# Kernel optimization log

Measured on AMD Instinct MI355X. Metric: run time of the kernel, lower is better.

## Reference

```python
import jax, jax.numpy as jnp
import numpy as np

B, N, M = 4, 50000, 256
BIN_MIN, BIN_MAX = -3.0, 3.0


def setup_inputs() -> dict:
    key = jax.random.key(0)
    kx, ky = jax.random.split(key)
    x_coords = jax.random.normal(kx, (B, N), dtype=jnp.float32)
    y_coords = jax.random.normal(ky, (B, N), dtype=jnp.float32)
    bins = jnp.linspace(BIN_MIN, BIN_MAX, M, dtype=jnp.float32)
    return {"x_coords": x_coords, "y_coords": y_coords, "bins": bins}


def reference(x_coords, y_coords, bins):
    # bandwidth defaults to bin resolution (bins[1] - bins[0])
    bandwidth = bins[1] - bins[0]
    # per-axis Gaussian kernel values: (B, N, M)
    kx = jnp.exp(-0.5 * jnp.square((x_coords[..., None] - bins) / bandwidth))
    ky = jnp.exp(-0.5 * jnp.square((y_coords[..., None] - bins) / bandwidth))
    # joint kernel values reduced over particles: (B, M, M)
    joint = jnp.einsum("bni,bnj->bij", kx, ky)
    norm = jnp.sum(joint, axis=(-2, -1), keepdims=True) + 1e-10
    return joint / norm
```

## Files before the change

kernel.cpp:

```cpp
#include <hip/hip_runtime.h>


#define B_     4
#define N_     50000
#define M_     256
#define BK     64
#define NCH    48
#define KSTEPS 17
#define KCH    (KSTEPS * BK)
#define LDKB   80
#define ROWS   129
#define AXB    (ROWS * LDKB)
#define BUFB   (2 * AXB)
#define BLOCK  256
#define WINB   7
#define CS2    0.72134752f
#define HINV   0.36787944f

#if __has_builtin(__builtin_amdgcn_exp2f)
  #define EXP2(t) __builtin_amdgcn_exp2f(t)
#else
  #define EXP2(t) exp2f(t)
#endif

typedef __attribute__((ext_vector_type(4))) int i32x4;

__device__ __forceinline__ unsigned short bf16ru(float f) {
    return (unsigned short)((__builtin_bit_cast(unsigned, f) + 0x8000u) >> 16);
}
__device__ __forceinline__ float bf2f(unsigned short u) {
    return __builtin_bit_cast(float, ((unsigned)u) << 16);
}

template<int MT, int R0, bool SCAT>
__device__ __forceinline__ float chunk_loop(
    char* __restrict__ tb, const float* __restrict__ coord,
    int k0, int rowlo, int colbase, float bin0, float invbw,
    int ilo, int jlo, int wj, int lm, int quad, int tid,
    unsigned short* __restrict__ pb)
{
    i32x4 acc[MT][4];
    #pragma unroll
    for (int mt = 0; mt < MT; ++mt)
        #pragma unroll
        for (int nt = 0; nt < 4; ++nt) acc[mt][nt] = i32x4{0, 0, 0, 0};

    int ps0 = 1 << 20, ps1 = 1 << 20;

    float v0 = 3.0e30f, vnext = 3.0e30f;
    if (SCAT) {
        const int kcol = tid & 63;
        const int ka = k0 + kcol;       if (ka  < N_) v0    = coord[ka];
        const int kb2 = k0 + BK + kcol; if (kb2 < N_) vnext = coord[kb2];
    }
    __syncthreads();

    if (SCAT) {
        const float u  = (v0 - bin0) * invbw;
        const float st = rintf(u) - 3.0f;
        const float d0 = u - st;
        float E = 127.0f * EXP2(-CS2 * d0 * d0);
        float G = EXP2(fmaf(d0 + d0, CS2, -CS2));
        int rr = (int)st - rowlo;
        ps0 = rr;
        const int dmp = colbase + 128 * LDKB;
        #pragma unroll
        for (int j = 0; j < WINB; ++j) {
            tb[((unsigned)rr < 128u) ? (colbase + rr * LDKB) : dmp] =
                (char)(int)(E + 0.5f);
            E *= G; G *= HINV; ++rr;
        }
    }
    __syncthreads();

    for (int ks = 0; ks < KSTEPS; ++ks) {
        const int q = ks & 1;
        float vpre = 3.0e30f;
        if (SCAT && (ks + 2) < KSTEPS) {
            const int ka = k0 + (ks + 2) * BK + (tid & 63);
            if (ka < N_) vpre = coord[ka];
        }
        if (SCAT && (ks + 1) < KSTEPS) {
            const int qn  = q ^ 1;
            const int bqn = qn * BUFB + colbase;
            const int dmp = bqn + 128 * LDKB;
            const int ps  = qn ? ps1 : ps0;
            if (ps < (1 << 19)) {
                #pragma unroll
                for (int j = 0; j < WINB; ++j) {
                    const int rr = ps + j;
                    tb[((unsigned)rr < 128u) ? (bqn + rr * LDKB) : dmp] = 0;
                }
            }
            const float u  = (vnext - bin0) * invbw;
            const float st = rintf(u) - 3.0f;
            const float d0 = u - st;
            float E = 127.0f * EXP2(-CS2 * d0 * d0);
            float G = EXP2(fmaf(d0 + d0, CS2, -CS2));
            int rr = (int)st - rowlo;
            if (qn) ps1 = rr; else ps0 = rr;
            #pragma unroll
            for (int j = 0; j < WINB; ++j) {
                tb[((unsigned)rr < 128u) ? (bqn + rr * LDKB) : dmp] =
                    (char)(int)(E + 0.5f);
                E *= G; G *= HINV; ++rr;
            }
        }
        vnext = vpre;

        const char* bufA = tb + q * BUFB;
        const char* bufB = tb + q * BUFB + AXB;
        i32x4 af[MT], bfr[4];
        #pragma unroll
        for (int t4 = 0; t4 < MT; ++t4)
            af[t4] = *(const i32x4*)(bufA + (R0 + t4 * 16 + lm) * LDKB + quad * 16);
        #pragma unroll
        for (int t4 = 0; t4 < 4; ++t4)
            bfr[t4] = *(const i32x4*)(bufB + (wj + t4 * 16 + lm) * LDKB + quad * 16);
        #pragma unroll
        for (int mt = 0; mt < MT; ++mt)
            #pragma unroll
            for (int nt = 0; nt < 4; ++nt)
                acc[mt][nt] = __builtin_amdgcn_mfma_i32_16x16x64_i8(
                    af[mt], bfr[nt], acc[mt][nt], 0, 0, 0);
        __syncthreads();
    }

    float tsum = 0.f;
    #pragma unroll
    for (int mt = 0; mt < MT; ++mt) {
        const int row0 = ilo + R0 + mt * 16 + quad * 4;
        #pragma unroll
        for (int nt = 0; nt < 4; ++nt) {
            const int col = jlo + wj + nt * 16 + lm;
            const i32x4 a = acc[mt][nt];
            #pragma unroll
            for (int e = 0; e < 4; ++e) {
                const float v = (float)a[e];
                pb[(size_t)(row0 + e) * M_ + col] = bf16ru(v);
                tsum += v;
            }
        }
    }
    return tsum;
}

__global__ __launch_bounds__(BLOCK) void kde_gemm(
    const float* __restrict__ xs, const float* __restrict__ ys,
    const float* __restrict__ bins, unsigned short* __restrict__ partial,
    float* __restrict__ ws2, int wide)
{
    __shared__ __align__(16) char tiles[2][2][ROWS][LDKB];
    __shared__ float sred[4];

    const int tid   = threadIdx.x;
    const int tile  = blockIdx.x;
    const int chunk = blockIdx.y;
    const int b     = blockIdx.z;

    const int ilo = (tile & 1) * 128;
    const int jlo = (tile >> 1) * 128;
    const float bin0  = bins[0];
    const float invbw = 1.0f / (bins[1] - bin0);

    {
        int4* za = (int4*)&tiles[0][0][0][0];
        const int4 z4 = {0, 0, 0, 0};
        for (int t = tid; t < (int)(sizeof(tiles) / 16); t += BLOCK) za[t] = z4;
    }

    const int  axis    = (tid >> 6) & 1;
    const int  rowlo   = axis ? jlo : ilo;
    const int  colbase = axis * AXB + (tid & 63);
    const float* coord = (axis ? ys : xs) + b * N_;
    const int  k0 = chunk * KCH;
    char* const tb = &tiles[0][0][0][0];

    const int w    = tid >> 6;
    const int wj   = (w & 1) * 64;
    const int lane = tid & 63;
    const int lm   = lane & 15;
    const int quad = lane >> 4;
    unsigned short* pb = partial + (((size_t)chunk * B_ + b) << 16);

    float tsum;
    if (w < 2)
        tsum = chunk_loop<3, 0, true >(tb, coord, k0, rowlo, colbase, bin0, invbw,
                                       ilo, jlo, wj, lm, quad, tid, pb);
    else
        tsum = chunk_loop<5, 48, false>(tb, coord, k0, rowlo, colbase, bin0, invbw,
                                       ilo, jlo, wj, lm, quad, tid, pb);

    #pragma unroll
    for (int off = 32; off; off >>= 1) tsum += __shfl_xor(tsum, off);
    if (lane == 0) sred[w] = tsum;
    __syncthreads();
    if (tid == 0) {
        const float bsum = sred[0] + sred[1] + sred[2] + sred[3];
        if (wide) {
            const int bid = (b * NCH + chunk) * 4 + tile;
            ws2[bid] = bsum;
        } else {
            atomicAdd(&ws2[b], bsum);
        }
    }
}

__global__ __launch_bounds__(BLOCK) void kde_tail(
    const unsigned short* __restrict__ partial, const float* __restrict__ ws2,
    float* __restrict__ out, int wide)
{
    __shared__ float sred[4];
    __shared__ float snorm;
    const int tid = threadIdx.x;
    const int cellIdx = blockIdx.x * BLOCK + tid;
    const int bb = cellIdx >> 14;
    const int cb = cellIdx & 16383;

    float nrm;
    if (wide) {
        float t = (tid < 4 * NCH) ? ws2[bb * 4 * NCH + tid] : 0.f;
        #pragma unroll
        for (int off = 32; off; off >>= 1) t += __shfl_xor(t, off);
        if ((tid & 63) == 0) sred[tid >> 6] = t;
        __syncthreads();
        if (tid == 0) snorm = sred[0] + sred[1] + sred[2] + sred[3];
        __syncthreads();
        nrm = snorm;
    } else {
        nrm = ws2[bb];
    }

    float4 a = {0.f, 0.f, 0.f, 0.f};
    #pragma unroll 4
    for (int c = 0; c < NCH; ++c) {
        const ushort4 v = *(const ushort4*)(partial +
            (((size_t)c * B_ + bb) << 16) + (size_t)cb * 4);
        a.x += bf2f(v.x); a.y += bf2f(v.y); a.z += bf2f(v.z); a.w += bf2f(v.w);
    }
    const float sc = 1.0f / (nrm + 1e-10f);
    a.x *= sc; a.y *= sc; a.z *= sc; a.w *= sc;
    ((float4*)out)[cellIdx] = a;
}

extern "C" void kernel_launch(void* const* d_in, const int* in_sizes, int n_in,
                              void* d_out, int out_size, void* d_ws, size_t ws_size,
                              hipStream_t stream)
{
    const float* xs   = (const float*)d_in[0];
    const float* ys   = (const float*)d_in[1];
    const float* bins = (const float*)d_in[2];
    float* out = (float*)d_out;
    unsigned short* partial = (unsigned short*)d_ws;
    const size_t PSZ = (size_t)NCH * B_ * M_ * M_ * sizeof(unsigned short);
    float* ws2 = (float*)((char*)d_ws + PSZ);

    const int wide = (ws_size >= PSZ + 4096) ? 1 : 0;
    if (!wide) hipMemsetAsync(ws2, 0, 4 * sizeof(float), stream);

    kde_gemm<<<dim3(4, NCH, B_), dim3(BLOCK), 0, stream>>>(
        xs, ys, bins, partial, ws2, wide);
    kde_tail<<<dim3(B_ * M_ * M_ / (4 * BLOCK)), dim3(BLOCK), 0, stream>>>(
        partial, ws2, out, wide);
}
```

Measured before the change: 89.46 us.

## Widen GEMM block to 128x256 output tile with 8 waves and more K-chunks

Each block now computes a 128x256 slab of the joint histogram with 512 threads (8 waves, each doing a 64x64 sub-tile), instead of 128x128 tiles with 256 threads. Two waves still scatter the Gaussian window values into LDS for the x rows and the full y axis, so the x-side scatter is shared across twice as many output columns. NCH rises to 64 and KSTEPS drops to 13, giving more, shorter chunks. The cost is a larger partial-sum buffer that the tail kernel must reduce, plus bigger LDS use per block.

```diff
diff --git a/kernel.cpp b/kernel.cpp
--- a/kernel.cpp
+++ b/kernel.cpp
@@ -5,14 +5,16 @@
 #define N_     50000
 #define M_     256
 #define BK     64
-#define NCH    48
-#define KSTEPS 17
+#define NCH    64
+#define KSTEPS 13
 #define KCH    (KSTEPS * BK)
 #define LDKB   80
-#define ROWS   129
-#define AXB    (ROWS * LDKB)
-#define BUFB   (2 * AXB)
-#define BLOCK  256
+#define AROWS  128
+#define BROWS  256
+#define AXA    ((AROWS + 1) * LDKB)
+#define AXBB   ((BROWS + 1) * LDKB)
+#define BUFB   (AXA + AXBB)
+#define BLOCK  512
 #define WINB   7
 #define CS2    0.72134752f
 #define HINV   0.36787944f
@@ -32,30 +34,61 @@
     return __builtin_bit_cast(float, ((unsigned)u) << 16);
 }
 
-template<int MT, int R0, bool SCAT>
-__device__ __forceinline__ float chunk_loop(
-    char* __restrict__ tb, const float* __restrict__ coord,
-    int k0, int rowlo, int colbase, float bin0, float invbw,
-    int ilo, int jlo, int wj, int lm, int quad, int tid,
-    unsigned short* __restrict__ pb)
+__global__ __launch_bounds__(BLOCK, 4) void kde_gemm(
+    const float* __restrict__ xs, const float* __restrict__ ys,
+    const float* __restrict__ bins, unsigned short* __restrict__ partial,
+    float* __restrict__ ws2, int wide)
 {
-    i32x4 acc[MT][4];
+    __shared__ __align__(16) char tiles[2 * BUFB];
+    __shared__ float sred[8];
+
+    const int tid   = threadIdx.x;
+    const int itile = blockIdx.x;
+    const int chunk = blockIdx.y;
+    const int b     = blockIdx.z;
+
+    const int ilo = itile * 128;
+    const float bin0  = bins[0];
+    const float invbw = 1.0f / (bins[1] - bin0);
+
+    {
+        int4* za = (int4*)tiles;
+        const int4 z4 = {0, 0, 0, 0};
+        for (int t = tid; t < (2 * BUFB) / 16; t += BLOCK) za[t] = z4;
+    }
+
+    const int w    = tid >> 6;
+    const int lane = tid & 63;
+    const int lm   = lane & 15;
+    const int quad = lane >> 4;
+
+    const bool sc      = (w < 2);
+    const int  rowlo   = (w == 0) ? ilo : 0;
+    const unsigned clip = (w == 0) ? 128u : 256u;
+    const int  cb0     = ((w == 0) ? 0 : AXA) + lane;
+    const float* coord = ((w == 0) ? xs : ys) + b * N_;
+    const int  k0      = chunk * KCH;
+    char* const tb     = tiles;
+
+    const int R0 = (w >> 2) * 64;
+    const int wj = (w & 3) * 64;
+
+    i32x4 acc[4][4];
     #pragma unroll
-    for (int mt = 0; mt < MT; ++mt)
+    for (int mt = 0; mt < 4; ++mt)
         #pragma unroll
         for (int nt = 0; nt < 4; ++nt) acc[mt][nt] = i32x4{0, 0, 0, 0};
 
     int ps0 = 1 << 20, ps1 = 1 << 20;
 
     float v0 = 3.0e30f, vnext = 3.0e30f;
-    if (SCAT) {
-        const int kcol = tid & 63;
-        const int ka = k0 + kcol;       if (ka  < N_) v0    = coord[ka];
-        const int kb2 = k0 + BK + kcol; if (kb2 < N_) vnext = coord[kb2];
+    if (sc) {
+        const int ka = k0 + lane;       if (ka  < N_) v0    = coord[ka];
+        const int kb2 = k0 + BK + lane; if (kb2 < N_) vnext = coord[kb2];
     }
     __syncthreads();
 
-    if (SCAT) {
+    if (sc) {
         const float u  = (v0 - bin0) * invbw;
         const float st = rintf(u) - 3.0f;
         const float d0 = u - st;
@@ -63,10 +96,10 @@
         float G = EXP2(fmaf(d0 + d0, CS2, -CS2));
         int rr = (int)st - rowlo;
         ps0 = rr;
-        const int dmp = colbase + 128 * LDKB;
+        const int dmp = cb0 + (int)clip * LDKB;
         #pragma unroll
         for (int j = 0; j < WINB; ++j) {
-            tb[((unsigned)rr < 128u) ? (colbase + rr * LDKB) : dmp] =
+            tb[((unsigned)rr < clip) ? (cb0 + rr * LDKB) : dmp] =
                 (char)(int)(E + 0.5f);
             E *= G; G *= HINV; ++rr;
         }
@@ -76,20 +109,20 @@
     for (int ks = 0; ks < KSTEPS; ++ks) {
         const int q = ks & 1;
         float vpre = 3.0e30f;
-        if (SCAT && (ks + 2) < KSTEPS) {
-            const int ka = k0 + (ks + 2) * BK + (tid & 63);
+        if (sc && (ks + 2) < KSTEPS) {
+            const int ka = k0 + (ks + 2) * BK + lane;
             if (ka < N_) vpre = coord[ka];
         }
-        if (SCAT && (ks + 1) < KSTEPS) {
+        if (sc && (ks + 1) < KSTEPS) {
             const int qn  = q ^ 1;
-            const int bqn = qn * BUFB + colbase;
-            const int dmp = bqn + 128 * LDKB;
+            const int bqn = qn * BUFB + cb0;
+            const int dmp = bqn + (int)clip * LDKB;
             const int ps  = qn ? ps1 : ps0;
             if (ps < (1 << 19)) {
                 #pragma unroll
                 for (int j = 0; j < WINB; ++j) {
                     const int rr = ps + j;
-                    tb[((unsigned)rr < 128u) ? (bqn + rr * LDKB) : dmp] = 0;
+                    tb[((unsigned)rr < clip) ? (bqn + rr * LDKB) : dmp] = 0;
                 }
             }
             const float u  = (vnext - bin0) * invbw;
@@ -101,7 +134,7 @@
             if (qn) ps1 = rr; else ps0 = rr;
             #pragma unroll
             for (int j = 0; j < WINB; ++j) {
-                tb[((unsigned)rr < 128u) ? (bqn + rr * LDKB) : dmp] =
+                tb[((unsigned)rr < clip) ? (bqn + rr * LDKB) : dmp] =
                     (char)(int)(E + 0.5f);
                 E *= G; G *= HINV; ++rr;
             }
@@ -109,16 +142,16 @@
         vnext = vpre;
 
         const char* bufA = tb + q * BUFB;
-        const char* bufB = tb + q * BUFB + AXB;
-        i32x4 af[MT], bfr[4];
-        #pragma unroll
-        for (int t4 = 0; t4 < MT; ++t4)
+        const char* bufB = tb + q * BUFB + AXA;
+        i32x4 af[4], bfr[4];
+        #pragma unroll
+        for (int t4 = 0; t4 < 4; ++t4)
             af[t4] = *(const i32x4*)(bufA + (R0 + t4 * 16 + lm) * LDKB + quad * 16);
         #pragma unroll
         for (int t4 = 0; t4 < 4; ++t4)
             bfr[t4] = *(const i32x4*)(bufB + (wj + t4 * 16 + lm) * LDKB + quad * 16);
         #pragma unroll
-        for (int mt = 0; mt < MT; ++mt)
+        for (int mt = 0; mt < 4; ++mt)
             #pragma unroll
             for (int nt = 0; nt < 4; ++nt)
                 acc[mt][nt] = __builtin_amdgcn_mfma_i32_16x16x64_i8(
@@ -127,78 +160,35 @@
     }
 
     float tsum = 0.f;
-    #pragma unroll
-    for (int mt = 0; mt < MT; ++mt) {
-        const int row0 = ilo + R0 + mt * 16 + quad * 4;
-        #pragma unroll
-        for (int nt = 0; nt < 4; ++nt) {
-            const int col = jlo + wj + nt * 16 + lm;
-            const i32x4 a = acc[mt][nt];
+    {
+        unsigned short* pb = partial + (((size_t)chunk * B_ + b) << 16);
+        #pragma unroll
+        for (int mt = 0; mt < 4; ++mt) {
+            const int row0 = ilo + R0 + mt * 16 + quad * 4;
             #pragma unroll
-            for (int e = 0; e < 4; ++e) {
-                const float v = (float)a[e];
-                pb[(size_t)(row0 + e) * M_ + col] = bf16ru(v);
-                tsum += v;
+            for (int nt = 0; nt < 4; ++nt) {
+                const int col = wj + nt * 16 + lm;
+                const i32x4 a = acc[mt][nt];
+                #pragma unroll
+                for (int e = 0; e < 4; ++e) {
+                    const float v = (float)a[e];
+                    pb[(size_t)(row0 + e) * M_ + col] = bf16ru(v);
+                    tsum += v;
+                }
             }
         }
     }
-    return tsum;
-}
-
-__global__ __launch_bounds__(BLOCK) void kde_gemm(
-    const float* __restrict__ xs, const float* __restrict__ ys,
-    const float* __restrict__ bins, unsigned short* __restrict__ partial,
-    float* __restrict__ ws2, int wide)
-{
-    __shared__ __align__(16) char tiles[2][2][ROWS][LDKB];
-    __shared__ float sred[4];
-
-    const int tid   = threadIdx.x;
-    const int tile  = blockIdx.x;
-    const int chunk = blockIdx.y;
-    const int b     = blockIdx.z;
-
-    const int ilo = (tile & 1) * 128;
-    const int jlo = (tile >> 1) * 128;
-    const float bin0  = bins[0];
-    const float invbw = 1.0f / (bins[1] - bin0);
-
-    {
-        int4* za = (int4*)&tiles[0][0][0][0];
-        const int4 z4 = {0, 0, 0, 0};
-        for (int t = tid; t < (int)(sizeof(tiles) / 16); t += BLOCK) za[t] = z4;
-    }
-
-    const int  axis    = (tid >> 6) & 1;
-    const int  rowlo   = axis ? jlo : ilo;
-    const int  colbase = axis * AXB + (tid & 63);
-    const float* coord = (axis ? ys : xs) + b * N_;
-    const int  k0 = chunk * KCH;
-    char* const tb = &tiles[0][0][0][0];
-
-    const int w    = tid >> 6;
-    const int wj   = (w & 1) * 64;
-    const int lane = tid & 63;
-    const int lm   = lane & 15;
-    const int quad = lane >> 4;
-    unsigned short* pb = partial + (((size_t)chunk * B_ + b) << 16);
-
-    float tsum;
-    if (w < 2)
-        tsum = chunk_loop<3, 0, true >(tb, coord, k0, rowlo, colbase, bin0, invbw,
-                                       ilo, jlo, wj, lm, quad, tid, pb);
-    else
-        tsum = chunk_loop<5, 48, false>(tb, coord, k0, rowlo, colbase, bin0, invbw,
-                                       ilo, jlo, wj, lm, quad, tid, pb);
 
     #pragma unroll
     for (int off = 32; off; off >>= 1) tsum += __shfl_xor(tsum, off);
     if (lane == 0) sred[w] = tsum;
     __syncthreads();
     if (tid == 0) {
-        const float bsum = sred[0] + sred[1] + sred[2] + sred[3];
+        float bsum = 0.f;
+        #pragma unroll
+        for (int i = 0; i < 8; ++i) bsum += sred[i];
         if (wide) {
-            const int bid = (b * NCH + chunk) * 4 + tile;
+            const int bid = (b * NCH + chunk) * 2 + itile;
             ws2[bid] = bsum;
         } else {
             atomicAdd(&ws2[b], bsum);
@@ -206,20 +196,20 @@
     }
 }
 
-__global__ __launch_bounds__(BLOCK) void kde_tail(
+__global__ __launch_bounds__(256) void kde_tail(
     const unsigned short* __restrict__ partial, const float* __restrict__ ws2,
     float* __restrict__ out, int wide)
 {
     __shared__ float sred[4];
     __shared__ float snorm;
     const int tid = threadIdx.x;
-    const int cellIdx = blockIdx.x * BLOCK + tid;
+    const int cellIdx = blockIdx.x * 256 + tid;
     const int bb = cellIdx >> 14;
     const int cb = cellIdx & 16383;
 
     float nrm;
     if (wide) {
-        float t = (tid < 4 * NCH) ? ws2[bb * 4 * NCH + tid] : 0.f;
+        float t = (tid < 128) ? ws2[bb * 128 + tid] : 0.f;
         #pragma unroll
         for (int off = 32; off; off >>= 1) t += __shfl_xor(t, off);
         if ((tid & 63) == 0) sred[tid >> 6] = t;
@@ -258,8 +248,8 @@
     const int wide = (ws_size >= PSZ + 4096) ? 1 : 0;
     if (!wide) hipMemsetAsync(ws2, 0, 4 * sizeof(float), stream);
 
-    kde_gemm<<<dim3(4, NCH, B_), dim3(BLOCK), 0, stream>>>(
+    kde_gemm<<<dim3(2, NCH, B_), dim3(BLOCK), 0, stream>>>(
         xs, ys, bins, partial, ws2, wide);
-    kde_tail<<<dim3(B_ * M_ * M_ / (4 * BLOCK)), dim3(BLOCK), 0, stream>>>(
+    kde_tail<<<dim3(B_ * M_ * M_ / (4 * 256)), dim3(256), 0, stream>>>(
         partial, ws2, out, wide);
 }
```

After: 91.59 us. 2.4% more time.
